# Performance work log

Measured on AMD Instinct MI355X. Metric: run time of the kernel, lower is better.

The kernel has to match this reference:

```python
import jax, jax.numpy as jnp
import numpy as np
import math

_PI = math.pi

@jax.custom_vjp
def atan_spike(h):
    # Heaviside forward, ATan surrogate (alpha=2.0) backward
    return (h >= 0).astype(h.dtype)

def _atan_fwd(h):
    return (h >= 0).astype(h.dtype), h

def _atan_bwd(h, g):
    # d/dh [ (1/pi) atan(pi*h) + 1/2 ] = 1 / (1 + (pi*h)^2)
    return (g / (1.0 + (_PI * h) ** 2),)

atan_spike.defvjp(_atan_fwd, _atan_bwd)

def plif_scan(x, alpha, v_th):
    # x: [T, ...]; PLIF: v += alpha*(x - v); spike; hard reset to 0
    a = alpha.reshape(())
    def step(v, xt):
        v = v + a * (xt - v)
        s = atan_spike(v - v_th)
        v = v * (1.0 - s)
        return v, s
    v0 = jnp.zeros_like(x[0])
    _, spikes = jax.lax.scan(step, v0, x)
    return spikes

def setup_inputs() -> dict:
    key = jax.random.key(0)
    k1, k2, k3 = jax.random.split(key, 3)
    T, B, N, D, H = 4, 8, 1024, 512, 2048
    x = jax.random.normal(k1, (T, B, N, D), dtype=jnp.float32)
    W1 = jax.random.normal(k2, (H, D), dtype=jnp.float32) * (1.0 / math.sqrt(D))
    W2 = jax.random.normal(k3, (D, H), dtype=jnp.float32) * (1.0 / math.sqrt(H))
    alpha1 = jnp.full((1,), 0.5, dtype=jnp.float32)  # 1/tau, tau=2.0
    alpha2 = jnp.full((1,), 0.5, dtype=jnp.float32)
    return {"x": x, "W1": W1, "W2": W2, "alpha1": alpha1, "alpha2": alpha2}

def reference(x, W1, W2, alpha1, alpha2):
    V_TH = 1.0
    h = jnp.einsum('tbnd,hd->tbnh', x, W1)      # fc1 (no bias)
    s1 = plif_scan(h, alpha1, V_TH)             # PLIF neuron 1
    y = jnp.einsum('tbnh,dh->tbnd', s1, W2)     # fc2 (no bias)
    s2 = plif_scan(y, alpha2, V_TH)             # PLIF neuron 2
    return s2
```

## Files before the change

kernel.cpp:

```cpp
#include <hip/hip_runtime.h>

#define T_  4
#define BN_ 8192
#define D_  512
#define H_  2048

typedef float f4 __attribute__((ext_vector_type(4)));
typedef float f32x4 __attribute__((ext_vector_type(4)));
typedef _Float16 f16x8 __attribute__((ext_vector_type(8)));

__device__ __forceinline__ void split8(const f4 u0, const f4 u1, f16x8& hi, f16x8& lo) {
#pragma unroll
    for (int i = 0; i < 4; ++i) {
        _Float16 a = (_Float16)u0[i]; hi[i]     = a; lo[i]     = (_Float16)(u0[i] - (float)a);
        _Float16 b = (_Float16)u1[i]; hi[4 + i] = b; lo[4 + i] = (_Float16)(u1[i] - (float)b);
    }
}

__device__ __forceinline__ void spikes4_to_f16(unsigned b, unsigned& lo, unsigned& hi) {
    const unsigned p0 = (b & 0xFFu) | ((b & 0xFF00u) << 8);
    const unsigned p1 = ((b >> 16) & 0xFFu) | ((b >> 8) & 0xFF0000u);
    lo = p0 * 0x3C00u;
    hi = p1 * 0x3C00u;
}

__device__ __forceinline__ void glds16(const void* g, void* l) {
    __builtin_amdgcn_global_load_lds((const __attribute__((address_space(1))) unsigned int*)g,
                                     (__attribute__((address_space(3))) unsigned int*)l, 16, 0, 0);
}

__global__ __launch_bounds__(256)
void k_split(const float* __restrict__ x, _Float16* __restrict__ xs)
{
    const int b     = blockIdx.x;
    const int t     = b & 3;
    const int k0B   = (b >> 2) & 15;
    const int bnB64 = b >> 6;
    const int kg    = threadIdx.x & 3;
    const int row64 = threadIdx.x >> 2;

    const float* src = x + ((size_t)t * BN_ + bnB64 * 64 + row64) * D_ + k0B * 32 + kg * 8;
    const f4 u0 = *(const f4*)src;
    const f4 u1 = *(const f4*)(src + 4);
    f16x8 hi, lo;
    split8(u0, u1, hi, lo);

    const int bnB32 = bnB64 * 2 + (row64 >> 5);
    const int r     = row64 & 31;
    const size_t base = (size_t)(bnB32 * 16 + k0B) * 8192 + t * 2048;
    *(f16x8*)&xs[base +        kg * 256 + r * 8] = hi;
    *(f16x8*)&xs[base + 1024 + kg * 256 + r * 8] = lo;
}

__global__ __launch_bounds__(256)
void k_splitW(const float* __restrict__ W1, _Float16* __restrict__ w1s)
{
    const int gid = blockIdx.x * 256 + threadIdx.x;
    const int col = gid & 127;
    const int kg  = (gid >> 7) & 3;
    const int kb  = (gid >> 9) & 15;
    const int h0b = gid >> 13;

    const float* src = W1 + (size_t)(h0b * 128 + col) * D_ + kb * 32 + kg * 8;
    const f4 u0 = *(const f4*)src;
    const f4 u1 = *(const f4*)(src + 4);
    f16x8 hi, lo;
    split8(u0, u1, hi, lo);

    const size_t base = (size_t)(h0b * 16 + kb) * 8192;
    *(f16x8*)&w1s[base +        kg * 1024 + col * 8] = hi;
    *(f16x8*)&w1s[base + 4096 + kg * 1024 + col * 8] = lo;
}

__global__ __launch_bounds__(256)
void k_splitW2(const float* __restrict__ W2, _Float16* __restrict__ w2s)
{
    const int gid = blockIdx.x * 256 + threadIdx.x;
    const int col = gid & 127;
    const int kg  = (gid >> 7) & 3;
    const int kb  = (gid >> 9) & 63;
    const int d0b = gid >> 15;

    const float* src = W2 + (size_t)(d0b * 128 + col) * H_ + kb * 32 + kg * 8;
    const f4 u0 = *(const f4*)src;
    const f4 u1 = *(const f4*)(src + 4);
    f16x8 hi, lo;
    split8(u0, u1, hi, lo);

    const size_t base = (size_t)(d0b * 64 + kb) * 8192;
    *(f16x8*)&w2s[base +        kg * 1024 + col * 8] = hi;
    *(f16x8*)&w2s[base + 4096 + kg * 1024 + col * 8] = lo;
}

__global__ __launch_bounds__(256, 3)
void k_fc1b(const _Float16* __restrict__ xs, const _Float16* __restrict__ w1s,
            const float* __restrict__ alphap, unsigned char* __restrict__ s1)
{
    __shared__ _Float16 Ab[3][T_][2][4][32][8];

    const int tid  = threadIdx.x;
    const int lane = tid & 63;
    const int w    = tid >> 6;
    const int wc   = w * 32;

    const int gid   = blockIdx.x;
    const int panel = gid >> 8;
    const int h0i   = (gid >> 4) & 15;
    const int bnL   = gid & 15;
    const int bnB   = panel * 16 + bnL;
    const int bn0   = bnB * 32;
    const int h0    = h0i * 128;

    const int l15 = lane & 15;
    const int kgl = lane >> 4;
    const int lq  = kgl * 4;

    const float a1v = alphap[0];

    f32x4 acc[T_][2][2];
#pragma unroll
    for (int t = 0; t < T_; ++t)
#pragma unroll
        for (int m = 0; m < 2; ++m)
#pragma unroll
            for (int n = 0; n < 2; ++n) acc[t][m][n] = (f32x4){0.f, 0.f, 0.f, 0.f};

    const char* xbase = (const char*)xs + (size_t)bnB * 16 * 16384;
    const _Float16* bl = w1s + (size_t)h0i * (16 * 8192)
                             + (size_t)kgl * 1024 + (size_t)(wc + l15) * 8;

#define FC1_GLDS(BUF, KB)                                                        \
    {                                                                            \
        const char* cb_ = xbase + (size_t)(KB) * 16384;                          \
        _Float16* lA_ = &Ab[BUF][0][0][0][0][0];                                 \
        _Pragma("unroll")                                                        \
        for (int i_ = 0; i_ < 4; ++i_) {                                         \
            const int s_ = i_ * 4 + w;                                           \
            glds16(cb_ + s_ * 1024 + lane * 16, lA_ + s_ * 512);                 \
        }                                                                        \
    }

#define FC1_BLOAD(KB, B0, B1)                                                    \
    {                                                                            \
        const _Float16* bp_ = bl + (size_t)(KB) * 8192;                          \
        B0[0] = *(const f16x8*)(bp_);                                            \
        B0[1] = *(const f16x8*)(bp_ + 128);                                      \
        B1[0] = *(const f16x8*)(bp_ + 4096);                                     \
        B1[1] = *(const f16x8*)(bp_ + 4096 + 128);                               \
    }

#define FC1_COMPUTE(BUF, B0, B1)                                                 \
    _Pragma("unroll")                                                            \
    for (int t_ = 0; t_ < T_; ++t_)                                              \
        _Pragma("unroll")                                                        \
        for (int m_ = 0; m_ < 2; ++m_) {                                         \
            const f16x8 a0_ = *(const f16x8*)&Ab[BUF][t_][0][kgl][m_ * 16 + l15][0]; \
            const f16x8 a1_ = *(const f16x8*)&Ab[BUF][t_][1][kgl][m_ * 16 + l15][0]; \
            _Pragma("unroll")                                                    \
            for (int n_ = 0; n_ < 2; ++n_) {                                     \
                acc[t_][m_][n_] = __builtin_amdgcn_mfma_f32_16x16x32_f16(a0_, B0[n_], acc[t_][m_][n_], 0, 0, 0); \
                acc[t_][m_][n_] = __builtin_amdgcn_mfma_f32_16x16x32_f16(a0_, B1[n_], acc[t_][m_][n_], 0, 0, 0); \
                acc[t_][m_][n_] = __builtin_amdgcn_mfma_f32_16x16x32_f16(a1_, B0[n_], acc[t_][m_][n_], 0, 0, 0); \
            }                                                                    \
        }

#define FC1_SB __builtin_amdgcn_sched_barrier(0);
#define FC1_WAIT(N) asm volatile("s_waitcnt vmcnt(" #N ")" ::: "memory");

#define FC1_PHASE(P, SC0, SC1, SP0, SP1, BUFC, BUFP, PRE, WN)                    \
    __builtin_amdgcn_s_barrier();                                                \
    FC1_SB                                                                       \
    if (PRE) {                                                                   \
        FC1_BLOAD((P) + 2, SP0, SP1)                                             \
        FC1_SB                                                                   \
        FC1_GLDS(BUFP, (P) + 2)                                                  \
        FC1_SB                                                                   \
    }                                                                            \
    FC1_WAIT(WN)                                                                 \
    FC1_SB                                                                       \
    FC1_COMPUTE(BUFC, SC0, SC1)

    f16x8 b0A[2], b0B[2], b1A[2], b1B[2], b2A[2], b2B[2];

    FC1_BLOAD(0, b0A, b0B)
    FC1_SB
    FC1_GLDS(0, 0)
    FC1_SB
    FC1_BLOAD(1, b1A, b1B)
    FC1_SB
    FC1_GLDS(1, 1)
    FC1_SB

#pragma unroll 1
    for (int i = 0; i < 4; ++i) {
        const int p = 3 * i;
        FC1_PHASE(p,     b0A, b0B, b2A, b2B, 0, 2, 1, 16)
        FC1_PHASE(p + 1, b1A, b1B, b0A, b0B, 1, 0, 1, 16)
        FC1_PHASE(p + 2, b2A, b2B, b1A, b1B, 2, 1, 1, 16)
    }
    FC1_PHASE(12, b0A, b0B, b2A, b2B, 0, 2, 1, 16)
    FC1_PHASE(13, b1A, b1B, b0A, b0B, 1, 0, 1, 16)
    FC1_PHASE(14, b2A, b2B, b0A, b0B, 2, 0, 0, 8)
    FC1_PHASE(15, b0A, b0B, b0A, b0B, 0, 0, 0, 0)

#pragma unroll
    for (int m = 0; m < 2; ++m)
#pragma unroll
        for (int n = 0; n < 2; ++n)
#pragma unroll
            for (int q = 0; q < 4; ++q) {
                float v = 0.f;
#pragma unroll
                for (int t = 0; t < T_; ++t) {
                    v = v + a1v * (acc[t][m][n][q] - v);
                    const bool sp = (v >= 1.0f);
                    s1[((size_t)t * BN_ + bn0 + m * 16 + lq + q) * H_ +
                       (h0 + wc + n * 16 + l15)] = sp ? (unsigned char)1 : (unsigned char)0;
                    if (sp) v = 0.f;
                }
            }
}

__global__ __launch_bounds__(256, 2)
void k_fc2b(const unsigned char* __restrict__ s1, const _Float16* __restrict__ w2s,
            const float* __restrict__ alphap, float* __restrict__ out)
{
    __shared__ _Float16 A2[2][T_][4][64][8];

    const int tid  = threadIdx.x;
    const int lane = tid & 63;
    const int w    = tid >> 6;
    const int wr   = (w >> 1) * 32;
    const int wc   = (w & 1) * 64;
    const int bn0  = blockIdx.x * 64;
    const int d0i  = blockIdx.y;
    const int d0   = d0i * 128;

    const int l15 = lane & 15;
    const int kgl = lane >> 4;
    const int lq  = kgl * 4;

    const int at   = w;
    const int arow = lane;

    const float a2v = alphap[0];

    f32x4 acc[T_][2][4];
#pragma unroll
    for (int t = 0; t < T_; ++t)
#pragma unroll
        for (int m = 0; m < 2; ++m)
#pragma unroll
            for (int n = 0; n < 4; ++n) acc[t][m][n] = (f32x4){0.f, 0.f, 0.f, 0.f};

    const unsigned char* ap = s1 + ((size_t)at * BN_ + bn0 + arow) * H_;
    const _Float16* bl = w2s + (size_t)d0i * (64 * 8192)
                             + (size_t)kgl * 1024 + (size_t)(wc + l15) * 8;

#define FC2_ACONV_WRITE(BUF, R0, R1)                                             \
    {                                                                            \
        unsigned v_[8];                                                          \
        spikes4_to_f16(R0.x, v_[0], v_[1]); spikes4_to_f16(R0.y, v_[2], v_[3]);  \
        spikes4_to_f16(R0.z, v_[4], v_[5]); spikes4_to_f16(R0.w, v_[6], v_[7]);  \
        *(uint4*)&A2[BUF][at][0][arow][0] = *(const uint4*)&v_[0];               \
        *(uint4*)&A2[BUF][at][1][arow][0] = *(const uint4*)&v_[4];               \
        spikes4_to_f16(R1.x, v_[0], v_[1]); spikes4_to_f16(R1.y, v_[2], v_[3]);  \
        spikes4_to_f16(R1.z, v_[4], v_[5]); spikes4_to_f16(R1.w, v_[6], v_[7]);  \
        *(uint4*)&A2[BUF][at][2][arow][0] = *(const uint4*)&v_[0];               \
        *(uint4*)&A2[BUF][at][3][arow][0] = *(const uint4*)&v_[4];               \
    }

#define FC2_BLOAD(KB, B0, B1)                                                    \
    {                                                                            \
        const _Float16* bp_ = bl + (size_t)(KB) * 8192;                          \
        _Pragma("unroll")                                                        \
        for (int n_ = 0; n_ < 4; ++n_) {                                         \
            B0[n_] = *(const f16x8*)(bp_ + n_ * 128);                            \
            B1[n_] = *(const f16x8*)(bp_ + 4096 + n_ * 128);                     \
        }                                                                        \
    }

    f16x8 bc0[4], bc1[4], bpA0[4], bpA1[4];

    {
        const uint4 r0 = *(const uint4*)(ap);
        const uint4 r1 = *(const uint4*)(ap + 16);
        FC2_ACONV_WRITE(0, r0, r1)
        FC2_BLOAD(0, bc0, bc1)
    }
    __syncthreads();

    int cur = 0;
    for (int kb = 0; kb < 64; ++kb) {
        uint4 r0, r1;
        if (kb < 63) {
            r0 = *(const uint4*)(ap + (kb + 1) * 32);
            r1 = *(const uint4*)(ap + (kb + 1) * 32 + 16);
            FC2_BLOAD(kb + 1, bpA0, bpA1)
        }

#pragma unroll
        for (int t = 0; t < T_; ++t)
#pragma unroll
            for (int m = 0; m < 2; ++m) {
                const f16x8 af = *(const f16x8*)&A2[cur][t][kgl][wr + m * 16 + l15][0];
#pragma unroll
                for (int n = 0; n < 4; ++n) {
                    acc[t][m][n] = __builtin_amdgcn_mfma_f32_16x16x32_f16(af, bc0[n], acc[t][m][n], 0, 0, 0);
                    acc[t][m][n] = __builtin_amdgcn_mfma_f32_16x16x32_f16(af, bc1[n], acc[t][m][n], 0, 0, 0);
                }
            }

        if (kb < 63) {
            FC2_ACONV_WRITE(cur ^ 1, r0, r1)
        }
        __syncthreads();
        if (kb < 63) {
#pragma unroll
            for (int n = 0; n < 4; ++n) { bc0[n] = bpA0[n]; bc1[n] = bpA1[n]; }
        }
        cur ^= 1;
    }

#pragma unroll
    for (int m = 0; m < 2; ++m)
#pragma unroll
        for (int n = 0; n < 4; ++n)
#pragma unroll
            for (int q = 0; q < 4; ++q) {
                float v = 0.f;
#pragma unroll
                for (int t = 0; t < T_; ++t) {
                    v = v + a2v * (acc[t][m][n][q] - v);
                    const bool sp = (v >= 1.0f);
                    out[((size_t)t * BN_ + bn0 + wr + m * 16 + lq + q) * D_ +
                        (d0 + wc + n * 16 + l15)] = sp ? 1.0f : 0.0f;
                    if (sp) v = 0.f;
                }
            }
}

__global__ __launch_bounds__(256, 2)
void k_fc2(const unsigned char* __restrict__ s1, const float* __restrict__ W2,
           const float* __restrict__ alphap, float* __restrict__ out)
{
    __shared__ _Float16 A2[2][4][4][64][8];
    __shared__ _Float16 B2[2][2][4][128][8];

    const int tid  = threadIdx.x;
    const int lane = tid & 63;
    const int w    = tid >> 6;
    const int wr   = (w >> 1) * 32;
    const int wc   = (w & 1) * 64;
    const int bn0  = blockIdx.x * 64;
    const int d0   = blockIdx.y * 128;

    const int l15 = lane & 15;
    const int kgl = lane >> 4;
    const int lq  = kgl * 4;

    const int bcol = tid & 127;
    const int bkh  = tid >> 7;
    const int at   = tid >> 6;
    const int arow = lane;

    const float a2v = alphap[0];

    f32x4 acc[T_][2][4];
#pragma unroll
    for (int t = 0; t < T_; ++t)
#pragma unroll
        for (int m = 0; m < 2; ++m)
#pragma unroll
            for (int n = 0; n < 4; ++n) acc[t][m][n] = (f32x4){0.f, 0.f, 0.f, 0.f};

    const unsigned char* ap = s1 + ((size_t)at * BN_ + bn0 + arow) * H_;
    const float*         wp0 = W2 + (size_t)(d0 + bcol) * H_ + bkh * 16;

    {
        const uint4 r0 = *(const uint4*)(ap);
        const uint4 r1 = *(const uint4*)(ap + 16);
        unsigned v[8];
        spikes4_to_f16(r0.x, v[0], v[1]); spikes4_to_f16(r0.y, v[2], v[3]);
        spikes4_to_f16(r0.z, v[4], v[5]); spikes4_to_f16(r0.w, v[6], v[7]);
        *(uint4*)&A2[0][at][0][arow][0] = *(const uint4*)&v[0];
        *(uint4*)&A2[0][at][1][arow][0] = *(const uint4*)&v[4];
        spikes4_to_f16(r1.x, v[0], v[1]); spikes4_to_f16(r1.y, v[2], v[3]);
        spikes4_to_f16(r1.z, v[4], v[5]); spikes4_to_f16(r1.w, v[6], v[7]);
        *(uint4*)&A2[0][at][2][arow][0] = *(const uint4*)&v[0];
        *(uint4*)&A2[0][at][3][arow][0] = *(const uint4*)&v[4];

        const f4 w0 = *(const f4*)wp0, w1 = *(const f4*)(wp0 + 4);
        const f4 w2 = *(const f4*)(wp0 + 8), w3 = *(const f4*)(wp0 + 12);
        f16x8 hA, lA, hB, lB;
        split8(w0, w1, hA, lA); split8(w2, w3, hB, lB);
        *(f16x8*)&B2[0][0][2 * bkh][bcol][0]     = hA;
        *(f16x8*)&B2[0][0][2 * bkh + 1][bcol][0] = hB;
        *(f16x8*)&B2[0][1][2 * bkh][bcol][0]     = lA;
        *(f16x8*)&B2[0][1][2 * bkh + 1][bcol][0] = lB;
    }
    __syncthreads();

    int cur = 0;
    for (int kb = 0; kb < 64; ++kb) {
        uint4 r0, r1; f4 w0, w1, w2, w3;
        if (kb < 63) {
            r0 = *(const uint4*)(ap + (kb + 1) * 32);
            r1 = *(const uint4*)(ap + (kb + 1) * 32 + 16);
            const float* wp = wp0 + (kb + 1) * 32;
            w0 = *(const f4*)wp;       w1 = *(const f4*)(wp + 4);
            w2 = *(const f4*)(wp + 8); w3 = *(const f4*)(wp + 12);
        }

        f16x8 bf0[4], bf1[4];
#pragma unroll
        for (int n = 0; n < 4; ++n) {
            bf0[n] = *(const f16x8*)&B2[cur][0][kgl][wc + n * 16 + l15][0];
            bf1[n] = *(const f16x8*)&B2[cur][1][kgl][wc + n * 16 + l15][0];
        }
#pragma unroll
        for (int t = 0; t < T_; ++t)
#pragma unroll
            for (int m = 0; m < 2; ++m) {
                const f16x8 af = *(const f16x8*)&A2[cur][t][kgl][wr + m * 16 + l15][0];
#pragma unroll
                for (int n = 0; n < 4; ++n) {
                    acc[t][m][n] = __builtin_amdgcn_mfma_f32_16x16x32_f16(af, bf0[n], acc[t][m][n], 0, 0, 0);
                    acc[t][m][n] = __builtin_amdgcn_mfma_f32_16x16x32_f16(af, bf1[n], acc[t][m][n], 0, 0, 0);
                }
            }

        if (kb < 63) {
            unsigned v[8];
            spikes4_to_f16(r0.x, v[0], v[1]); spikes4_to_f16(r0.y, v[2], v[3]);
            spikes4_to_f16(r0.z, v[4], v[5]); spikes4_to_f16(r0.w, v[6], v[7]);
            *(uint4*)&A2[cur ^ 1][at][0][arow][0] = *(const uint4*)&v[0];
            *(uint4*)&A2[cur ^ 1][at][1][arow][0] = *(const uint4*)&v[4];
            spikes4_to_f16(r1.x, v[0], v[1]); spikes4_to_f16(r1.y, v[2], v[3]);
            spikes4_to_f16(r1.z, v[4], v[5]); spikes4_to_f16(r1.w, v[6], v[7]);
            *(uint4*)&A2[cur ^ 1][at][2][arow][0] = *(const uint4*)&v[0];
            *(uint4*)&A2[cur ^ 1][at][3][arow][0] = *(const uint4*)&v[4];

            f16x8 hA, lA, hB, lB;
            split8(w0, w1, hA, lA); split8(w2, w3, hB, lB);
            *(f16x8*)&B2[cur ^ 1][0][2 * bkh][bcol][0]     = hA;
            *(f16x8*)&B2[cur ^ 1][0][2 * bkh + 1][bcol][0] = hB;
            *(f16x8*)&B2[cur ^ 1][1][2 * bkh][bcol][0]     = lA;
            *(f16x8*)&B2[cur ^ 1][1][2 * bkh + 1][bcol][0] = lB;
        }
        __syncthreads();
        cur ^= 1;
    }

#pragma unroll
    for (int m = 0; m < 2; ++m)
#pragma unroll
        for (int n = 0; n < 4; ++n)
#pragma unroll
            for (int q = 0; q < 4; ++q) {
                float v = 0.f;
#pragma unroll
                for (int t = 0; t < T_; ++t) {
                    v = v + a2v * (acc[t][m][n][q] - v);
                    const bool sp = (v >= 1.0f);
                    out[((size_t)t * BN_ + bn0 + wr + m * 16 + lq + q) * D_ +
                        (d0 + wc + n * 16 + l15)] = sp ? 1.0f : 0.0f;
                    if (sp) v = 0.f;
                }
            }
}

extern "C" void kernel_launch(void* const* d_in, const int* in_sizes, int n_in,
                              void* d_out, int out_size, void* d_ws, size_t ws_size,
                              hipStream_t stream) {
    const float* x      = (const float*)d_in[0];
    const float* W1     = (const float*)d_in[1];
    const float* W2     = (const float*)d_in[2];
    const float* alpha1 = (const float*)d_in[3];
    const float* alpha2 = (const float*)d_in[4];
    float* out = (float*)d_out;

    unsigned char* s1 = (unsigned char*)d_ws;
    _Float16* xs = (_Float16*)d_out;
    const size_t S1_BYTES  = (size_t)T_ * BN_ * H_;
    const size_t W1S_BYTES = (size_t)H_ * D_ * 2 * sizeof(_Float16);
    const size_t W2S_BYTES = (size_t)D_ * H_ * 2 * sizeof(_Float16);

    k_split<<<dim3(8192), dim3(256), 0, stream>>>(x, xs);

    _Float16* w1s = (_Float16*)((char*)d_ws + S1_BYTES);
    k_splitW<<<dim3(512), dim3(256), 0, stream>>>(W1, w1s);
    k_fc1b<<<dim3(4096), dim3(256), 0, stream>>>(xs, w1s, alpha1, s1);

    if (ws_size >= S1_BYTES + W1S_BYTES + W2S_BYTES) {
        _Float16* w2s = (_Float16*)((char*)d_ws + S1_BYTES + W1S_BYTES);
        k_splitW2<<<dim3(512), dim3(256), 0, stream>>>(W2, w2s);
        k_fc2b<<<dim3(128, 4), dim3(256), 0, stream>>>(s1, w2s, alpha2, out);
    } else {
        k_fc2<<<dim3(128, 4), dim3(256), 0, stream>>>(s1, W2, alpha2, out);
    }
}
```

Baseline: 297.3 us.

## Remap fc1 warps to timesteps and stage PLIF epilogue through LDS

The fc1 kernel now gives each warp one timestep and all 128 output columns, instead of splitting the 128 columns across warps for all four timesteps. Each warp loads the full B fragments (8 per half) into registers and reuses them across its rows, so per-warp global B traffic goes up while A reads shrink to one timestep slice. The software pipeline changes to a B-register double buffer with three A LDS buffers. Accumulators are written to a 64KB LDS exchange so each thread can run the PLIF recurrence over time and store packed 8-byte spike rows instead of scattered single bytes. Occupancy drops from 3 to 2 blocks per CU because of higher register and LDS use.

```diff
diff --git a/kernel.cpp b/kernel.cpp
--- a/kernel.cpp
+++ b/kernel.cpp
@@ -92,16 +92,15 @@
     *(f16x8*)&w2s[base + 4096 + kg * 1024 + col * 8] = lo;
 }
 
-__global__ __launch_bounds__(256, 3)
-void k_fc1b(const _Float16* __restrict__ xs, const _Float16* __restrict__ w1s,
+__global__ __launch_bounds__(256, 2)
+void k_fc1c(const _Float16* __restrict__ xs, const _Float16* __restrict__ w1s,
             const float* __restrict__ alphap, unsigned char* __restrict__ s1)
 {
-    __shared__ _Float16 Ab[3][T_][2][4][32][8];
+    __shared__ __align__(16) unsigned char LDSBUF[65536];
 
     const int tid  = threadIdx.x;
     const int lane = tid & 63;
     const int w    = tid >> 6;
-    const int wc   = w * 32;
 
     const int gid   = blockIdx.x;
     const int panel = gid >> 8;
@@ -117,108 +116,150 @@
 
     const float a1v = alphap[0];
 
-    f32x4 acc[T_][2][2];
-#pragma unroll
-    for (int t = 0; t < T_; ++t)
-#pragma unroll
-        for (int m = 0; m < 2; ++m)
-#pragma unroll
-            for (int n = 0; n < 2; ++n) acc[t][m][n] = (f32x4){0.f, 0.f, 0.f, 0.f};
+    f32x4 acc[2][8];
+#pragma unroll
+    for (int m = 0; m < 2; ++m)
+#pragma unroll
+        for (int n = 0; n < 8; ++n) acc[m][n] = (f32x4){0.f, 0.f, 0.f, 0.f};
 
     const char* xbase = (const char*)xs + (size_t)bnB * 16 * 16384;
     const _Float16* bl = w1s + (size_t)h0i * (16 * 8192)
-                             + (size_t)kgl * 1024 + (size_t)(wc + l15) * 8;
+                             + (size_t)kgl * 1024 + (size_t)l15 * 8;
 
 #define FC1_GLDS(BUF, KB)                                                        \
     {                                                                            \
         const char* cb_ = xbase + (size_t)(KB) * 16384;                          \
-        _Float16* lA_ = &Ab[BUF][0][0][0][0][0];                                 \
         _Pragma("unroll")                                                        \
         for (int i_ = 0; i_ < 4; ++i_) {                                         \
             const int s_ = i_ * 4 + w;                                           \
-            glds16(cb_ + s_ * 1024 + lane * 16, lA_ + s_ * 512);                 \
+            glds16(cb_ + s_ * 1024 + lane * 16, LDSBUF + (BUF) * 16384 + s_ * 1024); \
         }                                                                        \
     }
 
 #define FC1_BLOAD(KB, B0, B1)                                                    \
     {                                                                            \
         const _Float16* bp_ = bl + (size_t)(KB) * 8192;                          \
-        B0[0] = *(const f16x8*)(bp_);                                            \
-        B0[1] = *(const f16x8*)(bp_ + 128);                                      \
-        B1[0] = *(const f16x8*)(bp_ + 4096);                                     \
-        B1[1] = *(const f16x8*)(bp_ + 4096 + 128);                               \
+        _Pragma("unroll")                                                        \
+        for (int n_ = 0; n_ < 8; ++n_) {                                         \
+            B0[n_] = *(const f16x8*)(bp_ + n_ * 128);                            \
+            B1[n_] = *(const f16x8*)(bp_ + 4096 + n_ * 128);                     \
+        }                                                                        \
     }
 
 #define FC1_COMPUTE(BUF, B0, B1)                                                 \
     _Pragma("unroll")                                                            \
-    for (int t_ = 0; t_ < T_; ++t_)                                              \
+    for (int m_ = 0; m_ < 2; ++m_) {                                             \
+        const f16x8 a0_ = *(const f16x8*)(LDSBUF + (BUF) * 16384 + w * 4096 +    \
+                                          kgl * 512 + (m_ * 16 + l15) * 16);     \
+        const f16x8 a1_ = *(const f16x8*)(LDSBUF + (BUF) * 16384 + w * 4096 + 2048 + \
+                                          kgl * 512 + (m_ * 16 + l15) * 16);     \
         _Pragma("unroll")                                                        \
-        for (int m_ = 0; m_ < 2; ++m_) {                                         \
-            const f16x8 a0_ = *(const f16x8*)&Ab[BUF][t_][0][kgl][m_ * 16 + l15][0]; \
-            const f16x8 a1_ = *(const f16x8*)&Ab[BUF][t_][1][kgl][m_ * 16 + l15][0]; \
-            _Pragma("unroll")                                                    \
-            for (int n_ = 0; n_ < 2; ++n_) {                                     \
-                acc[t_][m_][n_] = __builtin_amdgcn_mfma_f32_16x16x32_f16(a0_, B0[n_], acc[t_][m_][n_], 0, 0, 0); \
-                acc[t_][m_][n_] = __builtin_amdgcn_mfma_f32_16x16x32_f16(a0_, B1[n_], acc[t_][m_][n_], 0, 0, 0); \
-                acc[t_][m_][n_] = __builtin_amdgcn_mfma_f32_16x16x32_f16(a1_, B0[n_], acc[t_][m_][n_], 0, 0, 0); \
-            }                                                                    \
-        }
+        for (int n_ = 0; n_ < 8; ++n_) {                                         \
+            acc[m_][n_] = __builtin_amdgcn_mfma_f32_16x16x32_f16(a0_, B0[n_], acc[m_][n_], 0, 0, 0); \
+            acc[m_][n_] = __builtin_amdgcn_mfma_f32_16x16x32_f16(a0_, B1[n_], acc[m_][n_], 0, 0, 0); \
+            acc[m_][n_] = __builtin_amdgcn_mfma_f32_16x16x32_f16(a1_, B0[n_], acc[m_][n_], 0, 0, 0); \
+        }                                                                        \
+    }
 
 #define FC1_SB __builtin_amdgcn_sched_barrier(0);
 #define FC1_WAIT(N) asm volatile("s_waitcnt vmcnt(" #N ")" ::: "memory");
 
-#define FC1_PHASE(P, SC0, SC1, SP0, SP1, BUFC, BUFP, PRE, WN)                    \
+#define FC1_PH(P, BUFC, C0, C1, BUFP, P0, P1)                                    \
     __builtin_amdgcn_s_barrier();                                                \
     FC1_SB                                                                       \
-    if (PRE) {                                                                   \
-        FC1_BLOAD((P) + 2, SP0, SP1)                                             \
-        FC1_SB                                                                   \
-        FC1_GLDS(BUFP, (P) + 2)                                                  \
-        FC1_SB                                                                   \
-    }                                                                            \
-    FC1_WAIT(WN)                                                                 \
+    FC1_BLOAD((P) + 1, P0, P1)                                                   \
     FC1_SB                                                                       \
-    FC1_COMPUTE(BUFC, SC0, SC1)
-
-    f16x8 b0A[2], b0B[2], b1A[2], b1B[2], b2A[2], b2B[2];
-
-    FC1_BLOAD(0, b0A, b0B)
-    FC1_SB
+    FC1_GLDS(BUFP, (P) + 2)                                                      \
+    FC1_SB                                                                       \
+    FC1_WAIT(24)                                                                 \
+    FC1_SB                                                                       \
+    FC1_COMPUTE(BUFC, C0, C1)
+
+    f16x8 bA0[8], bA1[8], bB0[8], bB1[8];
+
     FC1_GLDS(0, 0)
     FC1_SB
-    FC1_BLOAD(1, b1A, b1B)
+    FC1_BLOAD(0, bA0, bA1)
     FC1_SB
     FC1_GLDS(1, 1)
     FC1_SB
 
 #pragma unroll 1
-    for (int i = 0; i < 4; ++i) {
-        const int p = 3 * i;
-        FC1_PHASE(p,     b0A, b0B, b2A, b2B, 0, 2, 1, 16)
-        FC1_PHASE(p + 1, b1A, b1B, b0A, b0B, 1, 0, 1, 16)
-        FC1_PHASE(p + 2, b2A, b2B, b1A, b1B, 2, 1, 1, 16)
-    }
-    FC1_PHASE(12, b0A, b0B, b2A, b2B, 0, 2, 1, 16)
-    FC1_PHASE(13, b1A, b1B, b0A, b0B, 1, 0, 1, 16)
-    FC1_PHASE(14, b2A, b2B, b0A, b0B, 2, 0, 0, 8)
-    FC1_PHASE(15, b0A, b0B, b0A, b0B, 0, 0, 0, 0)
-
-#pragma unroll
-    for (int m = 0; m < 2; ++m)
-#pragma unroll
-        for (int n = 0; n < 2; ++n)
-#pragma unroll
-            for (int q = 0; q < 4; ++q) {
-                float v = 0.f;
-#pragma unroll
-                for (int t = 0; t < T_; ++t) {
-                    v = v + a1v * (acc[t][m][n][q] - v);
-                    const bool sp = (v >= 1.0f);
-                    s1[((size_t)t * BN_ + bn0 + m * 16 + lq + q) * H_ +
-                       (h0 + wc + n * 16 + l15)] = sp ? (unsigned char)1 : (unsigned char)0;
-                    if (sp) v = 0.f;
+    for (int i = 0; i < 2; ++i) {
+        const int p = 6 * i;
+        FC1_PH(p + 0, 0, bA0, bA1, 2, bB0, bB1)
+        FC1_PH(p + 1, 1, bB0, bB1, 0, bA0, bA1)
+        FC1_PH(p + 2, 2, bA0, bA1, 1, bB0, bB1)
+        FC1_PH(p + 3, 0, bB0, bB1, 2, bA0, bA1)
+        FC1_PH(p + 4, 1, bA0, bA1, 0, bB0, bB1)
+        FC1_PH(p + 5, 2, bB0, bB1, 1, bA0, bA1)
+    }
+    FC1_PH(12, 0, bA0, bA1, 2, bB0, bB1)
+    FC1_PH(13, 1, bB0, bB1, 0, bA0, bA1)
+    __builtin_amdgcn_s_barrier();
+    FC1_SB
+    FC1_BLOAD(15, bB0, bB1)
+    FC1_SB
+    FC1_WAIT(20)
+    FC1_SB
+    FC1_COMPUTE(2, bA0, bA1)
+    __builtin_amdgcn_s_barrier();
+    FC1_WAIT(0)
+    FC1_SB
+    FC1_COMPUTE(0, bB0, bB1)
+
+    __syncthreads();
+    {
+        float* EXw = (float*)LDSBUF + w * 4096;
+#pragma unroll
+        for (int m = 0; m < 2; ++m)
+#pragma unroll
+            for (int n = 0; n < 8; ++n)
+#pragma unroll
+                for (int q = 0; q < 4; ++q)
+                    EXw[(m * 16 + lq + q) * 128 + n * 16 + l15] = acc[m][n][q];
+    }
+    __syncthreads();
+    {
+        const float* EX = (const float*)LDSBUF;
+        const int rbase = w * 8 + kgl * 2;
+        const int c0    = l15 * 8;
+
+        float v[2][8];
+#pragma unroll
+        for (int j = 0; j < 2; ++j)
+#pragma unroll
+            for (int c = 0; c < 8; ++c) v[j][c] = 0.f;
+
+#pragma unroll
+        for (int t = 0; t < T_; ++t) {
+#pragma unroll
+            for (int j = 0; j < 2; ++j) {
+                const int r = rbase + j;
+                const f4 hA = *(const f4*)&EX[t * 4096 + r * 128 + c0];
+                const f4 hB = *(const f4*)&EX[t * 4096 + r * 128 + c0 + 4];
+                unsigned p0 = 0, p1 = 0;
+#pragma unroll
+                for (int c = 0; c < 4; ++c) {
+                    float vv = v[j][c];
+                    vv = vv + a1v * (hA[c] - vv);
+                    const bool sp = (vv >= 1.0f);
+                    p0 |= (sp ? 1u : 0u) << (8 * c);
+                    v[j][c] = sp ? 0.f : vv;
                 }
+#pragma unroll
+                for (int c = 0; c < 4; ++c) {
+                    float vv = v[j][4 + c];
+                    vv = vv + a1v * (hB[c] - vv);
+                    const bool sp = (vv >= 1.0f);
+                    p1 |= (sp ? 1u : 0u) << (8 * c);
+                    v[j][4 + c] = sp ? 0.f : vv;
+                }
+                uint2 st; st.x = p0; st.y = p1;
+                *(uint2*)&s1[((size_t)t * BN_ + bn0 + r) * H_ + h0 + c0] = st;
             }
+        }
+    }
 }
 
 __global__ __launch_bounds__(256, 2)
@@ -490,7 +531,7 @@
 
     _Float16* w1s = (_Float16*)((char*)d_ws + S1_BYTES);
     k_splitW<<<dim3(512), dim3(256), 0, stream>>>(W1, w1s);
-    k_fc1b<<<dim3(4096), dim3(256), 0, stream>>>(xs, w1s, alpha1, s1);
+    k_fc1c<<<dim3(4096), dim3(256), 0, stream>>>(xs, w1s, alpha1, s1);
 
     if (ws_size >= S1_BYTES + W1S_BYTES + W2S_BYTES) {
         _Float16* w2s = (_Float16*)((char*)d_ws + S1_BYTES + W1S_BYTES);
```

Measured after the change: 343.7 us. 15.6% more time.
